# Optimization experiments

Hardware: AMD Instinct MI355X
Metric: run time of the kernel (lower is better)

The kernel has to match this reference:

```python
import jax, jax.numpy as jnp
import numpy as np

ND, PD, NH = 256, 128, 8   # node_dim, pair_dim, n_head
HD = ND // NH              # head_dim = 32
N, L = 1, 256


def _inorm(x):
    # InstanceNorm2d (affine=False), x is NHWC: normalize per (N,C) over H,W
    m = jnp.mean(x, axis=(1, 2), keepdims=True)
    v = jnp.var(x, axis=(1, 2), keepdims=True)
    return (x - m) * jax.lax.rsqrt(v + 1e-5)


def _conv3x3(x, w, b):
    # w in torch OIHW layout -> HWIO; stride 1, padding 1 ('SAME')
    y = jax.lax.conv_general_dilated(x, jnp.transpose(w, (2, 3, 1, 0)), (1, 1), 'SAME',
                                     dimension_numbers=('NHWC', 'HWIO', 'NHWC'))
    return y + b


def _lrelu(x):
    return jnp.where(x >= 0, x, 0.01 * x)


def _ln(x, g, b):
    m = jnp.mean(x, axis=-1, keepdims=True)
    v = jnp.var(x, axis=-1, keepdims=True)
    return (x - m) * jax.lax.rsqrt(v + 1e-5) * g + b


def setup_inputs() -> dict:
    key = jax.random.key(0)
    ks = jax.random.split(key, 16)
    rn = lambda k, s: jax.random.normal(k, s, jnp.float32) * 0.02
    return dict(
        x=jax.random.normal(ks[0], (N, L, ND), jnp.float32),
        z=jax.random.normal(ks[1], (N, L, L, PD), jnp.float32),
        plddt=jax.random.uniform(ks[2], (N, L, L, 1), jnp.float32),
        Wq=rn(ks[3], (ND, ND)), Wk=rn(ks[4], (ND, ND)), Wv=rn(ks[5], (ND, ND)),
        Wp2a=rn(ks[6], (NH, PD)),
        conv_a_w=rn(ks[7], (NH, 2 * NH, 3, 3)), conv_a_b=jnp.zeros((NH,), jnp.float32),
        conv_p_w=rn(ks[8], (NH, NH + 1, 3, 3)), conv_p_b=jnp.zeros((NH,), jnp.float32),
        ln1_g=jnp.ones((NH * PD + ND,), jnp.float32), ln1_b=jnp.zeros((NH * PD + ND,), jnp.float32),
        lin1_w=rn(ks[9], (2 * ND, NH * PD + ND)), lin1_b=jnp.zeros((2 * ND,), jnp.float32),
        ln2_g=jnp.ones((2 * ND,), jnp.float32), ln2_b=jnp.zeros((2 * ND,), jnp.float32),
        lin2_w=rn(ks[10], (ND, 2 * ND)), lin2_b=jnp.zeros((ND,), jnp.float32),
        lnf_g=jnp.ones((ND,), jnp.float32), lnf_b=jnp.zeros((ND,), jnp.float32),
        conv_z_w=rn(ks[11], (PD, NH + PD, 3, 3)), conv_z_b=jnp.zeros((PD,), jnp.float32),
    )


def reference(x, z, plddt, Wq, Wk, Wv, Wp2a, conv_a_w, conv_a_b, conv_p_w, conv_p_b,
              ln1_g, ln1_b, lin1_w, lin1_b, ln2_g, ln2_b, lin2_w, lin2_b,
              lnf_g, lnf_b, conv_z_w, conv_z_b):
    n, l, _ = x.shape
    inv_sqrt_hd = np.float32(1.0 / np.sqrt(HD))
    # _node2alpha: per-head QK^T / sqrt(head_dim) -> (N,L,L,H)
    q = (x @ Wq.T).reshape(n, l, NH, HD)
    k = (x @ Wk.T).reshape(n, l, NH, HD)
    v = (x @ Wv.T).reshape(n, l, NH, HD)
    a_node = jnp.einsum('nihd,njhd->nijh', q, k) * inv_sqrt_hd
    # _pair2alpha
    a_pair = z @ Wp2a.T  # (N,L,L,H)
    # conv2dalpha: cat(pair, node) channels-last, InstanceNorm + Conv3x3 + LeakyReLU
    alpha = _lrelu(_conv3x3(_inorm(jnp.concatenate([a_pair, a_node], axis=-1)), conv_a_w, conv_a_b))
    # alpha_mask_plddt
    alpha = _lrelu(_conv3x3(_inorm(jnp.concatenate([alpha, plddt], axis=-1)), conv_p_w, conv_p_b))
    # _node_aggregation: (N,L,H,hd) head-major flatten -> (N,L,node_dim)
    node_from_node = jnp.einsum('nijh,njhd->nihd', alpha, v).reshape(n, l, ND)
    # _pair_aggregation: direct contraction over j (avoids (N,L,L,H,P) blowup)
    node_from_pair = jnp.einsum('nijh,nijp->nihp', alpha, z).reshape(n, l, NH * PD)
    # out_transform: LN -> Linear -> LN -> LeakyReLU -> Linear
    h = jnp.concatenate([node_from_pair, node_from_node], axis=-1)
    h = _ln(h, ln1_g, ln1_b)
    h = _ln(h @ lin1_w.T + lin1_b, ln2_g, ln2_b)
    x_out = _lrelu(h) @ lin2_w.T + lin2_b
    x_new = _ln(x + x_out, lnf_g, lnf_b)
    # alpha2pair
    z_new = _lrelu(_conv3x3(_inorm(jnp.concatenate([z, alpha], axis=-1)), conv_z_w, conv_z_b))
    return x_new, z_new
```

## Files before the change

### kernel.cpp

```cpp
#include <hip/hip_runtime.h>
#include <math.h>

#define LLEN 256
#define NDIM 256
#define NHEAD 8
#define HDIM 32
#define NPIX (LLEN*LLEN)

typedef __bf16 bf16x8 __attribute__((ext_vector_type(8)));
typedef float f32x4 __attribute__((ext_vector_type(4)));

constexpr size_t OFF_Q     = 0;
constexpr size_t OFF_K     = 65536;
constexpr size_t OFF_V     = 131072;
constexpr size_t OFF_CAT16 = 196608;
constexpr size_t OFF_H1B   = 196608;
constexpr size_t OFF_W1B   = 360448;
constexpr size_t OFF_A1    = 1245184;
constexpr size_t OFF_ALPHA = 1769472;
constexpr size_t OFF_AGG   = 2293760;
constexpr size_t OFF_Y     = 2621440;
constexpr size_t OFF_ST16  = 2752512;
constexpr size_t OFF_ST9   = 2752544;
constexpr size_t OFF_ST136 = 2752576;
constexpr size_t OFF_PART  = 2752864;
constexpr size_t OFF_PART2 = 2892128;
constexpr size_t OFF_WZB2  = 3031392;

__device__ inline unsigned short f2b(float x){
  union { float f; unsigned u; } a; a.f = x;
  unsigned r = a.u + 0x7fffu + ((a.u >> 16) & 1u);
  return (unsigned short)(r >> 16);
}

__global__ __launch_bounds__(256) void qkv_kernel(
    const float* __restrict__ x, const float* __restrict__ Wq,
    const float* __restrict__ Wk, const float* __restrict__ Wv,
    float* __restrict__ q, float* __restrict__ k, float* __restrict__ v){
  __shared__ __align__(16) float xs[8][256];
  int t = threadIdx.x;
  int i0 = blockIdx.x * 8;
  int m = blockIdx.y;
  const float* W = (m==0)?Wq:((m==1)?Wk:Wv);
  float* out = (m==0)?q:((m==1)?k:v);
  for (int idx = t; idx < 2048; idx += 256)
    xs[idx>>8][idx&255] = x[(size_t)i0*256 + idx];
  __syncthreads();
  float acc[8];
  #pragma unroll
  for (int r = 0; r < 8; r++) acc[r] = 0.f;
  const float4* wr = (const float4*)(W + (size_t)t*256);
  for (int kk = 0; kk < 64; ++kk){
    float4 w4 = wr[kk];
    #pragma unroll
    for (int r = 0; r < 8; r++){
      float4 xv = ((const float4*)xs[r])[kk];
      acc[r] += w4.x*xv.x + w4.y*xv.y + w4.z*xv.z + w4.w*xv.w;
    }
  }
  #pragma unroll
  for (int r = 0; r < 8; r++) out[(size_t)(i0+r)*256 + t] = acc[r];
}

__global__ __launch_bounds__(256) void cat16v3_kernel(
    const float* __restrict__ z, const float* __restrict__ qb,
    const float* __restrict__ kb, const float* __restrict__ Wp2a,
    float* __restrict__ cat16){
  __shared__ __align__(16) float zs2[32*132];
  __shared__ __align__(16) float ws2[8*132];
  int t = threadIdx.x;
  int pix0 = blockIdx.x * 32;
  int i = pix0 >> 8;
  int j0 = pix0 & 255;
  {
    int h = t >> 5, j = t & 31;
    float4 v = *(const float4*)(Wp2a + h*128 + j*4);
    *(float4*)(ws2 + h*132 + j*4) = v;
  }
  #pragma unroll
  for (int k = 0; k < 4; ++k){
    int idx = t + k*256;
    int pix = idx >> 5, j = idx & 31;
    float4 v = *(const float4*)(z + ((size_t)(pix0 + pix))*128 + j*4);
    *(float4*)(zs2 + pix*132 + j*4) = v;
  }
  __syncthreads();
  int p8 = t >> 3, h = t & 7;
  const float* zr = zs2 + p8*132;
  const float* wr = ws2 + h*132;
  float ap = 0.f;
  #pragma unroll 8
  for (int j = 0; j < 32; ++j){
    float4 a = *(const float4*)(zr + j*4);
    float4 b = *(const float4*)(wr + j*4);
    ap += a.x*b.x + a.y*b.y + a.z*b.z + a.w*b.w;
  }
  const float* qg = qb + (size_t)i*256 + h*32;
  const float* kg = kb + (size_t)(j0 + p8)*256 + h*32;
  float an = 0.f;
  #pragma unroll
  for (int d4 = 0; d4 < 8; ++d4){
    float4 a = *(const float4*)(qg + d4*4);
    float4 b = *(const float4*)(kg + d4*4);
    an += a.x*b.x + a.y*b.y + a.z*b.z + a.w*b.w;
  }
  an *= 0.17677669529663689f;
  int pix = pix0 + p8;
  cat16[(size_t)pix*16 + h] = ap;
  cat16[(size_t)pix*16 + 8 + h] = an;
}

__global__ __launch_bounds__(256) void statsA_z_kernel(
    const float* __restrict__ z, float* __restrict__ part, float* __restrict__ part2){
  __shared__ float4 sm[256], sq[256];
  int t = threadIdx.x, b = blockIdx.x;
  int c4 = t & 31, po = t >> 5;
  float4 s = {0,0,0,0}, q = {0,0,0,0};
  for (int g = 0; g < 8; ++g){
    int px = b*64 + po + g*8;
    float4 v = *(const float4*)(z + (size_t)px*128 + c4*4);
    s.x += v.x; s.y += v.y; s.z += v.z; s.w += v.w;
    q.x += v.x*v.x; q.y += v.y*v.y; q.z += v.z*v.z; q.w += v.w*v.w;
  }
  sm[t] = s; sq[t] = q;
  __syncthreads();
  if (t < 32){
    float4 S = sm[t], Q = sq[t];
    for (int p2 = 1; p2 < 8; ++p2){
      float4 a = sm[p2*32 + t], c = sq[p2*32 + t];
      S.x += a.x; S.y += a.y; S.z += a.z; S.w += a.w;
      Q.x += c.x; Q.y += c.y; Q.z += c.z; Q.w += c.w;
    }
    part [(size_t)(t*4+0)*1024 + b] = S.x; part [(size_t)(t*4+1)*1024 + b] = S.y;
    part [(size_t)(t*4+2)*1024 + b] = S.z; part [(size_t)(t*4+3)*1024 + b] = S.w;
    part2[(size_t)(t*4+0)*1024 + b] = Q.x; part2[(size_t)(t*4+1)*1024 + b] = Q.y;
    part2[(size_t)(t*4+2)*1024 + b] = Q.z; part2[(size_t)(t*4+3)*1024 + b] = Q.w;
  }
}

__global__ __launch_bounds__(256) void statsA_16_kernel(
    const float* __restrict__ src, float* __restrict__ part, float* __restrict__ part2){
  __shared__ float4 sm[256], sq[256];
  int t = threadIdx.x, b = blockIdx.x;
  int c4 = t & 3, po = t >> 2;
  float4 s = {0,0,0,0}, q = {0,0,0,0};
  for (int g = 0; g < 4; ++g){
    int px = b*256 + po + g*64;
    float4 v = *(const float4*)(src + (size_t)px*16 + c4*4);
    s.x += v.x; s.y += v.y; s.z += v.z; s.w += v.w;
    q.x += v.x*v.x; q.y += v.y*v.y; q.z += v.z*v.z; q.w += v.w*v.w;
  }
  sm[t] = s; sq[t] = q;
  __syncthreads();
  if (t < 4){
    float4 S = sm[t], Q = sq[t];
    for (int p2 = 1; p2 < 64; ++p2){
      float4 a = sm[p2*4 + t], c = sq[p2*4 + t];
      S.x += a.x; S.y += a.y; S.z += a.z; S.w += a.w;
      Q.x += c.x; Q.y += c.y; Q.z += c.z; Q.w += c.w;
    }
    part [(size_t)(t*4+0)*1024 + b] = S.x; part [(size_t)(t*4+1)*1024 + b] = S.y;
    part [(size_t)(t*4+2)*1024 + b] = S.z; part [(size_t)(t*4+3)*1024 + b] = S.w;
    part2[(size_t)(t*4+0)*1024 + b] = Q.x; part2[(size_t)(t*4+1)*1024 + b] = Q.y;
    part2[(size_t)(t*4+2)*1024 + b] = Q.z; part2[(size_t)(t*4+3)*1024 + b] = Q.w;
  }
}

__global__ __launch_bounds__(256) void statsA_s8_kernel(
    const float* __restrict__ src, float* __restrict__ part, float* __restrict__ part2,
    int coff){
  __shared__ float sm[256], sq[256];
  int t = threadIdx.x, b = blockIdx.x;
  int ch = t & 7, po = t >> 3;
  float s = 0.f, q = 0.f;
  for (int g = 0; g < 8; ++g){
    int px = b*256 + po + g*32;
    float v = src[(size_t)px*8 + ch];
    s += v; q += v*v;
  }
  sm[t] = s; sq[t] = q;
  __syncthreads();
  if (t < 8){
    float S = 0.f, Q = 0.f;
    for (int p2 = 0; p2 < 32; ++p2){ S += sm[p2*8 + t]; Q += sq[p2*8 + t]; }
    part [(size_t)(coff+t)*1024 + b] = S;
    part2[(size_t)(coff+t)*1024 + b] = Q;
  }
}

__device__ inline void block_reduce2(float& s, float& s2, float* red){
  int t = threadIdx.x;
  int lane = t & 63, wv = t >> 6;
  #pragma unroll
  for (int o = 32; o > 0; o >>= 1){ s += __shfl_down(s, o); s2 += __shfl_down(s2, o); }
  __syncthreads();
  if (lane == 0){ red[wv] = s; red[4+wv] = s2; }
  __syncthreads();
  s  = red[0]+red[1]+red[2]+red[3];
  s2 = red[4]+red[5]+red[6]+red[7];
}

__global__ __launch_bounds__(256) void statsA_s1_kernel(
    const float* __restrict__ src, float* __restrict__ part, float* __restrict__ part2,
    int coff){
  __shared__ float red[8];
  int t = threadIdx.x, b = blockIdx.x;
  float v = src[(size_t)b*256 + t];
  float s = v, q = v*v;
  block_reduce2(s, q, red);
  if (t == 0){ part[(size_t)coff*1024 + b] = s; part2[(size_t)coff*1024 + b] = q; }
}

__global__ __launch_bounds__(256) void statsB_kernel(
    const float* __restrict__ part, const float* __restrict__ part2,
    float* __restrict__ st, int C, int csplit, int nb_main, int nb_tail){
  __shared__ float red[8];
  int c = blockIdx.x, t = threadIdx.x;
  int nb = (c < csplit) ? nb_main : nb_tail;
  float s = 0.f, q = 0.f;
  for (int i = t; i < nb; i += 256){ s += part[(size_t)c*1024 + i]; q += part2[(size_t)c*1024 + i]; }
  block_reduce2(s, q, red);
  if (t == 0){
    float m = s * (1.f/NPIX);
    float var = q * (1.f/NPIX) - m*m;
    st[c] = m;
    st[C + c] = rsqrtf(var + 1e-5f);
  }
}

template<int CIN, int COUT>
__global__ __launch_bounds__(256) void conv_small5_kernel(
    const float* __restrict__ A, int Ca, const float* __restrict__ B, int Cb,
    const float* __restrict__ st, const float* __restrict__ w,
    const float* __restrict__ bias, float* __restrict__ out){
  constexpr int WD = 67;
  __shared__ float xn[3][CIN][WD];
  __shared__ float wsm[COUT*CIN*9];
  __shared__ float ms[CIN], isd[CIN], bs[COUT];
  int t = threadIdx.x;
  int i = blockIdx.x >> 2, chb = blockIdx.x & 3;
  int c0 = chb*64;
  if (t < CIN){ ms[t] = st[t]; isd[t] = st[CIN + t]; }
  if (t < COUT) bs[t] = bias[t];
  for (int idx = t; idx < COUT*CIN*9; idx += 256) wsm[idx] = w[idx];
  __syncthreads();
  constexpr int TOT = 66*CIN;
  for (int s = 0; s < 3; ++s){
    int ir = i - 1 + s;
    for (int idx = t; idx < TOT; idx += 256){
      int col = idx / CIN, c = idx - col*CIN;
      int gcol = c0 + col - 1;
      float vv = 0.f;
      if (ir >= 0 && ir < 256 && gcol >= 0 && gcol < 256){
        size_t pix = (size_t)ir*256 + gcol;
        float raw = (c < Ca) ? A[pix*Ca + c] : B[pix*Cb + (c - Ca)];
        vv = (raw - ms[c]) * isd[c];
      }
      xn[s][c][col] = vv;
    }
  }
  __syncthreads();
  int os = t >> 6, tc = t & 63;
  float a0 = bs[os*2], a1 = bs[os*2 + 1];
  #pragma unroll
  for (int kh = 0; kh < 3; ++kh){
    #pragma unroll
    for (int c = 0; c < CIN; ++c){
      float x0 = xn[kh][c][tc];
      float x1 = xn[kh][c][tc + 1];
      float x2 = xn[kh][c][tc + 2];
      const float* w0 = wsm + (((os*2+0)*CIN + c)*3 + kh)*3;
      const float* w1 = wsm + (((os*2+1)*CIN + c)*3 + kh)*3;
      a0 += x0*w0[0] + x1*w0[1] + x2*w0[2];
      a1 += x0*w1[0] + x1*w1[1] + x2*w1[2];
    }
  }
  a0 = (a0 >= 0.f) ? a0 : 0.01f*a0;
  a1 = (a1 >= 0.f) ? a1 : 0.01f*a1;
  float2 v2 = { a0, a1 };
  *(float2*)(out + ((size_t)(i*256 + c0 + tc))*COUT + os*2) = v2;
}

__global__ __launch_bounds__(512) void agg_kernel2(
    const float* __restrict__ alpha, const float* __restrict__ z,
    const float* __restrict__ v, float* __restrict__ agg){
  __shared__ float as[2048];
  __shared__ float pp[256][4];
  __shared__ float np[256];
  int i = blockIdx.x, t = threadIdx.x;
  for (int idx = t; idx < 2048; idx += 512) as[idx] = alpha[(size_t)i*2048 + idx];
  __syncthreads();
  int tt = t & 255, jh = t >> 8;
  int p = tt & 127, hh = tt >> 7;
  const float* zrow = z + (size_t)i*32768 + (size_t)jh*128*128;
  const float* ar0 = as + jh*128*8;
  float a0=0.f, a1=0.f, a2=0.f, a3=0.f;
  #pragma unroll 8
  for (int j = 0; j < 128; ++j){
    float zv = zrow[j*128 + p];
    const float* ar = ar0 + j*8 + hh*4;
    a0 += ar[0]*zv; a1 += ar[1]*zv; a2 += ar[2]*zv; a3 += ar[3]*zv;
  }
  int h = tt >> 5;
  float an = 0.f;
  const float* vrow = v + (size_t)jh*128*256;
  const float* ah0 = as + jh*128*8;
  #pragma unroll 8
  for (int j = 0; j < 128; ++j) an += ah0[j*8 + h]*vrow[j*256 + tt];
  if (jh == 1){
    pp[tt][0]=a0; pp[tt][1]=a1; pp[tt][2]=a2; pp[tt][3]=a3; np[tt]=an;
  }
  __syncthreads();
  if (jh == 0){
    a0 += pp[tt][0]; a1 += pp[tt][1]; a2 += pp[tt][2]; a3 += pp[tt][3];
    an += np[tt];
    size_t ob = (size_t)i*1280;
    agg[ob + (hh*4+0)*128 + p] = a0;
    agg[ob + (hh*4+1)*128 + p] = a1;
    agg[ob + (hh*4+2)*128 + p] = a2;
    agg[ob + (hh*4+3)*128 + p] = a3;
    agg[ob + 1024 + tt] = an;
  }
}

__global__ __launch_bounds__(256) void ln1_kernel(
    const float* __restrict__ agg,
    const float* __restrict__ ln1_g, const float* __restrict__ ln1_b,
    unsigned short* __restrict__ h1b){
  __shared__ float red[8];
  int i = blockIdx.x, t = threadIdx.x;
  float v[5], s = 0.f, s2 = 0.f;
  #pragma unroll
  for (int qq = 0; qq < 5; ++qq){
    v[qq] = agg[(size_t)i*1280 + qq*256 + t];
    s += v[qq]; s2 += v[qq]*v[qq];
  }
  block_reduce2(s, s2, red);
  float m = s*(1.f/1280.f), istd = rsqrtf(s2*(1.f/1280.f) - m*m + 1e-5f);
  #pragma unroll
  for (int qq = 0; qq < 5; ++qq){
    int kk = qq*256 + t;
    h1b[(size_t)i*1280 + kk] = f2b((v[qq] - m)*istd*ln1_g[kk] + ln1_b[kk]);
  }
}

__global__ __launch_bounds__(256) void w1_prep(const float* __restrict__ w,
                                               unsigned short* __restrict__ wb){
  int idx = (blockIdx.x*256 + threadIdx.x)*4;
  float4 v = *(const float4*)(w + idx);
  ushort4 u;
  u.x = f2b(v.x); u.y = f2b(v.y); u.z = f2b(v.z); u.w = f2b(v.w);
  *(ushort4*)(wb + idx) = u;
}

__global__ __launch_bounds__(256) void gemm1_kernel(
    const unsigned short* __restrict__ h1b, const unsigned short* __restrict__ w1b,
    const float* __restrict__ lin1_b, float* __restrict__ y){
  int t = threadIdx.x;
  int mb = blockIdx.x & 3, nb = blockIdx.x >> 2;
  int lane = t & 63, w = t >> 6;
  int li = lane & 15, lg = lane >> 4;
  int mh = w & 1, nh = w >> 1;
  int mbase = mb*64 + mh*32, nbase = nb*64 + nh*32;
  f32x4 acc[2][2];
  #pragma unroll
  for (int a = 0; a < 2; ++a)
    #pragma unroll
    for (int b = 0; b < 2; ++b) acc[a][b] = (f32x4){0.f,0.f,0.f,0.f};
  const unsigned short* ar0 = h1b + (size_t)(mbase + li)*1280 + lg*8;
  const unsigned short* ar1 = ar0 + 16*1280;
  const unsigned short* br0 = w1b + (size_t)(nbase + li)*1280 + lg*8;
  const unsigned short* br1 = br0 + 16*1280;
  #pragma unroll 4
  for (int ks = 0; ks < 40; ++ks){
    bf16x8 a0 = *(const bf16x8*)(ar0 + ks*32);
    bf16x8 a1 = *(const bf16x8*)(ar1 + ks*32);
    bf16x8 b0 = *(const bf16x8*)(br0 + ks*32);
    bf16x8 b1 = *(const bf16x8*)(br1 + ks*32);
    acc[0][0] = __builtin_amdgcn_mfma_f32_16x16x32_bf16(a0, b0, acc[0][0], 0,0,0);
    acc[0][1] = __builtin_amdgcn_mfma_f32_16x16x32_bf16(a0, b1, acc[0][1], 0,0,0);
    acc[1][0] = __builtin_amdgcn_mfma_f32_16x16x32_bf16(a1, b0, acc[1][0], 0,0,0);
    acc[1][1] = __builtin_amdgcn_mfma_f32_16x16x32_bf16(a1, b1, acc[1][1], 0,0,0);
  }
  #pragma unroll
  for (int mi = 0; mi < 2; ++mi){
    #pragma unroll
    for (int ni = 0; ni < 2; ++ni){
      int col = nbase + ni*16 + li;
      float bb = lin1_b[col];
      #pragma unroll
      for (int ri = 0; ri < 4; ++ri){
        int row = mbase + mi*16 + lg*4 + ri;
        y[(size_t)row*512 + col] = acc[mi][ni][ri] + bb;
      }
    }
  }
}

__global__ __launch_bounds__(256) void outB2_kernel(
    const float* __restrict__ y, const float* __restrict__ x,
    const float* __restrict__ ln2_g, const float* __restrict__ ln2_b,
    const float* __restrict__ lin2_w, const float* __restrict__ lin2_b,
    const float* __restrict__ lnf_g, const float* __restrict__ lnf_b,
    float* __restrict__ xout){
  __shared__ __align__(16) float h2[2][512];
  __shared__ float red[8];
  int t = threadIdx.x;
  int rb = blockIdx.x;
  for (int r = 0; r < 2; ++r){
    int i = rb*2 + r;
    float y0 = y[(size_t)i*512 + t], y1 = y[(size_t)i*512 + 256 + t];
    float s = y0 + y1, s2 = y0*y0 + y1*y1;
    block_reduce2(s, s2, red);
    float m = s*(1.f/512.f), istd = rsqrtf(s2*(1.f/512.f) - m*m + 1e-5f);
    float z0 = (y0 - m)*istd*ln2_g[t] + ln2_b[t];
    float z1 = (y1 - m)*istd*ln2_g[t+256] + ln2_b[t+256];
    h2[r][t]     = (z0 >= 0.f) ? z0 : 0.01f*z0;
    h2[r][t+256] = (z1 >= 0.f) ? z1 : 0.01f*z1;
  }
  __syncthreads();
  float acc[2];
  acc[0] = 0.f; acc[1] = 0.f;
  const float4* wr = (const float4*)(lin2_w + (size_t)t*512);
  #pragma unroll 4
  for (int kk = 0; kk < 128; ++kk){
    float4 w4 = wr[kk];
    #pragma unroll
    for (int r = 0; r < 2; ++r){
      float4 h = ((const float4*)h2[r])[kk];
      acc[r] += w4.x*h.x + w4.y*h.y + w4.z*h.z + w4.w*h.w;
    }
  }
  float bb = lin2_b[t];
  for (int r = 0; r < 2; ++r){
    int i = rb*2 + r;
    float xr = x[(size_t)i*256 + t] + acc[r] + bb;
    float s = xr, s2 = xr*xr;
    block_reduce2(s, s2, red);
    float m = s*(1.f/256.f), istd = rsqrtf(s2*(1.f/256.f) - m*m + 1e-5f);
    xout[(size_t)i*256 + t] = (xr - m)*istd*lnf_g[t] + lnf_b[t];
  }
}

__global__ __launch_bounds__(256) void wz_prep2(const float* __restrict__ w,
                                                unsigned short* __restrict__ wzb2){
  int idx = blockIdx.x*256 + threadIdx.x;
  if (idx >= 23040) return;
  int lane = idx & 63;
  int f = idx >> 6;
  int k = f % 5; int ft = f / 5; int tap = ft % 9; int ocb = ft / 9;
  int oc = ocb*16 + (lane & 15);
  int chb = k*32 + (lane >> 4)*8;
  unsigned short u[8];
  #pragma unroll
  for (int j = 0; j < 8; ++j){
    int ch = chb + j;
    float vv = (ch < 136) ? w[(size_t)oc*1224 + ch*9 + tap] : 0.f;
    u[j] = f2b(vv);
  }
  uint4 pk;
  pk.x = (unsigned)u[0] | ((unsigned)u[1]<<16);
  pk.y = (unsigned)u[2] | ((unsigned)u[3]<<16);
  pk.z = (unsigned)u[4] | ((unsigned)u[5]<<16);
  pk.w = (unsigned)u[6] | ((unsigned)u[7]<<16);
  *(uint4*)(wzb2 + (size_t)idx*8) = pk;
}

__global__ __launch_bounds__(256) void conv_z7_kernel(
    const float* __restrict__ z, const float* __restrict__ alpha,
    const float* __restrict__ st, const unsigned short* __restrict__ wzb2,
    const float* __restrict__ bias, float* __restrict__ out){
  __shared__ __align__(16) unsigned short xs[4*578*8];
  __shared__ float msp[153], isp[153];
  int t = threadIdx.x;
  int stripe = blockIdx.x & 7, rg = blockIdx.x >> 3;
  int i0 = rg*2, c0 = stripe*32;
  int lane = t & 63, w = t >> 6;
  int li = lane & 15, lg = lane >> 4;
  int wocb = w*2;
  if (t < 153){
    int cq = t/9, j = t - cq*9;
    bool vld = (j < 8);
    int ch = cq*8 + j;
    msp[t] = vld ? st[ch] : 0.f;
    isp[t] = vld ? st[136 + ch] : 0.f;
  }
  __syncthreads();
  for (int it = 0; it < 3; ++it){
    int cidx = t + it*256;
    int col = cidx / 17, cq = cidx - col*17;
    int gcol = c0 + col - 1;
    float mm[8], ss[8];
    #pragma unroll
    for (int j = 0; j < 8; ++j){ mm[j] = msp[cq*9 + j]; ss[j] = isp[cq*9 + j]; }
    if (cidx < 578){
      #pragma unroll
      for (int s = 0; s < 4; ++s){
        int ir = i0 - 1 + s;
        uint4 pk = {0u,0u,0u,0u};
        if (ir >= 0 && ir < 256 && gcol >= 0 && gcol < 256){
          const float* src = (cq < 16) ? (z + ((size_t)ir*256 + gcol)*128 + cq*8)
                                       : (alpha + ((size_t)ir*256 + gcol)*8);
          float4 r0 = *(const float4*)src;
          float4 r1 = *(const float4*)(src + 4);
          unsigned short u0 = f2b((r0.x - mm[0])*ss[0]);
          unsigned short u1 = f2b((r0.y - mm[1])*ss[1]);
          unsigned short u2 = f2b((r0.z - mm[2])*ss[2]);
          unsigned short u3 = f2b((r0.w - mm[3])*ss[3]);
          unsigned short u4 = f2b((r1.x - mm[4])*ss[4]);
          unsigned short u5 = f2b((r1.y - mm[5])*ss[5]);
          unsigned short u6 = f2b((r1.z - mm[6])*ss[6]);
          unsigned short u7 = f2b((r1.w - mm[7])*ss[7]);
          pk.x = (unsigned)u0 | ((unsigned)u1<<16);
          pk.y = (unsigned)u2 | ((unsigned)u3<<16);
          pk.z = (unsigned)u4 | ((unsigned)u5<<16);
          pk.w = (unsigned)u6 | ((unsigned)u7<<16);
        }
        *(uint4*)(xs + ((size_t)(s*578 + cidx))*8) = pk;
      }
    }
  }
  __syncthreads();

  f32x4 acc[2][2][2];
  #pragma unroll
  for (int r = 0; r < 2; ++r)
    #pragma unroll
    for (int m = 0; m < 2; ++m)
      #pragma unroll
      for (int o = 0; o < 2; ++o) acc[r][m][o] = (f32x4){0.f,0.f,0.f,0.f};

  for (int kh = 0; kh < 3; ++kh){
    for (int kw = 0; kw < 3; ++kw){
      int tap = kh*3 + kw;
      bf16x8 wf[5][2];
      #pragma unroll
      for (int k = 0; k < 5; ++k)
        #pragma unroll
        for (int o = 0; o < 2; ++o)
          wf[k][o] = *(const bf16x8*)(wzb2 + (size_t)((((wocb+o)*9 + tap)*5 + k)*64 + lane)*8);
      #pragma unroll
      for (int r = 0; r < 2; ++r){
        const unsigned short* sb = xs + (size_t)(r + kh)*578*8;
        #pragma unroll
        for (int k = 0; k < 5; ++k){
          int cq = (k < 4) ? (k*4 + lg) : 16;
          bf16x8 a0 = *(const bf16x8*)(sb + ((li+kw)*17 + cq)*8);
          bf16x8 a1 = *(const bf16x8*)(sb + ((li+kw+16)*17 + cq)*8);
          acc[r][0][0] = __builtin_amdgcn_mfma_f32_16x16x32_bf16(a0, wf[k][0], acc[r][0][0], 0,0,0);
          acc[r][0][1] = __builtin_amdgcn_mfma_f32_16x16x32_bf16(a0, wf[k][1], acc[r][0][1], 0,0,0);
          acc[r][1][0] = __builtin_amdgcn_mfma_f32_16x16x32_bf16(a1, wf[k][0], acc[r][1][0], 0,0,0);
          acc[r][1][1] = __builtin_amdgcn_mfma_f32_16x16x32_bf16(a1, wf[k][1], acc[r][1][1], 0,0,0);
        }
      }
    }
  }

  float b0 = bias[wocb*16 + li];
  float b1 = bias[(wocb+1)*16 + li];
  #pragma unroll
  for (int r = 0; r < 2; ++r){
    int i = i0 + r;
    #pragma unroll
    for (int m = 0; m < 2; ++m){
      #pragma unroll
      for (int ri = 0; ri < 4; ++ri){
        int px = m*16 + lg*4 + ri;
        size_t obase = ((size_t)(i*256 + c0 + px))*128;
        float v0 = acc[r][m][0][ri] + b0;
        float v1 = acc[r][m][1][ri] + b1;
        v0 = (v0 >= 0.f) ? v0 : 0.01f*v0;
        v1 = (v1 >= 0.f) ? v1 : 0.01f*v1;
        out[obase + wocb*16 + li]     = v0;
        out[obase + (wocb+1)*16 + li] = v1;
      }
    }
  }
}

extern "C" void kernel_launch(void* const* d_in, const int* in_sizes, int n_in,
                              void* d_out, int out_size, void* d_ws, size_t ws_size,
                              hipStream_t stream){
  const float* x        = (const float*)d_in[0];
  const float* z        = (const float*)d_in[1];
  const float* plddt    = (const float*)d_in[2];
  const float* Wq       = (const float*)d_in[3];
  const float* Wk       = (const float*)d_in[4];
  const float* Wv       = (const float*)d_in[5];
  const float* Wp2a     = (const float*)d_in[6];
  const float* conv_a_w = (const float*)d_in[7];
  const float* conv_a_b = (const float*)d_in[8];
  const float* conv_p_w = (const float*)d_in[9];
  const float* conv_p_b = (const float*)d_in[10];
  const float* ln1_g    = (const float*)d_in[11];
  const float* ln1_b    = (const float*)d_in[12];
  const float* lin1_w   = (const float*)d_in[13];
  const float* lin1_b   = (const float*)d_in[14];
  const float* ln2_g    = (const float*)d_in[15];
  const float* ln2_b    = (const float*)d_in[16];
  const float* lin2_w   = (const float*)d_in[17];
  const float* lin2_b   = (const float*)d_in[18];
  const float* lnf_g    = (const float*)d_in[19];
  const float* lnf_b    = (const float*)d_in[20];
  const float* conv_z_w = (const float*)d_in[21];
  const float* conv_z_b = (const float*)d_in[22];

  float* ws    = (float*)d_ws;
  float* q     = ws + OFF_Q;
  float* k     = ws + OFF_K;
  float* v     = ws + OFF_V;
  float* cat16 = ws + OFF_CAT16;
  float* a1    = ws + OFF_A1;
  float* alpha = ws + OFF_ALPHA;
  float* agg   = ws + OFF_AGG;
  float* y     = ws + OFF_Y;
  float* st16  = ws + OFF_ST16;
  float* st9   = ws + OFF_ST9;
  float* st136 = ws + OFF_ST136;
  float* part  = ws + OFF_PART;
  float* part2 = ws + OFF_PART2;
  unsigned short* wzb2 = (unsigned short*)(ws + OFF_WZB2);
  unsigned short* h1b  = (unsigned short*)(ws + OFF_H1B);
  unsigned short* w1b  = (unsigned short*)(ws + OFF_W1B);

  float* xout = (float*)d_out;
  float* zout = (float*)d_out + 65536;

  qkv_kernel<<<dim3(32,3), 256, 0, stream>>>(x, Wq, Wk, Wv, q, k, v);
  cat16v3_kernel<<<2048, 256, 0, stream>>>(z, q, k, Wp2a, cat16);
  statsA_16_kernel<<<256, 256, 0, stream>>>(cat16, part, part2);
  statsB_kernel<<<16, 256, 0, stream>>>(part, part2, st16, 16, 16, 256, 256);
  conv_small5_kernel<16,8><<<1024, 256, 0, stream>>>(cat16, 16, (const float*)nullptr, 0,
                                                     st16, conv_a_w, conv_a_b, a1);
  statsA_s8_kernel<<<256, 256, 0, stream>>>(a1, part, part2, 0);
  statsA_s1_kernel<<<256, 256, 0, stream>>>(plddt, part, part2, 8);
  statsB_kernel<<<9, 256, 0, stream>>>(part, part2, st9, 9, 9, 256, 256);
  conv_small5_kernel<9,8><<<1024, 256, 0, stream>>>(a1, 8, plddt, 1,
                                                    st9, conv_p_w, conv_p_b, alpha);
  agg_kernel2<<<256, 512, 0, stream>>>(alpha, z, v, agg);
  w1_prep<<<640, 256, 0, stream>>>(lin1_w, w1b);
  ln1_kernel<<<256, 256, 0, stream>>>(agg, ln1_g, ln1_b, h1b);
  gemm1_kernel<<<32, 256, 0, stream>>>(h1b, w1b, lin1_b, y);
  outB2_kernel<<<128, 256, 0, stream>>>(y, x, ln2_g, ln2_b, lin2_w, lin2_b,
                                        lnf_g, lnf_b, xout);
  statsA_z_kernel<<<1024, 256, 0, stream>>>(z, part, part2);
  statsA_s8_kernel<<<256, 256, 0, stream>>>(alpha, part, part2, 128);
  statsB_kernel<<<136, 256, 0, stream>>>(part, part2, st136, 136, 128, 1024, 256);
  wz_prep2<<<90, 256, 0, stream>>>(conv_z_w, wzb2);
  conv_z7_kernel<<<1024, 256, 0, stream>>>(z, alpha, st136, wzb2, conv_z_b, zout);
}
```

Baseline: 189.6 us.

## Fuse instance-norm partial statistics into producer kernels, drop separate stats passes

Per-block partial sums and squared sums for instance norm are now computed inside the cat16 and small-conv kernels from shared-memory tiles, instead of in separate statsA kernels that reread the intermediates. This removes four launches and their reads of cat16, a1, alpha and plddt. It adds a block barrier and a short serial reduction to the producer kernels. The scratch buffer for p16 is aliased onto the y region, which is safe only if y is written later.

Result: faster. 183.6 us (-3.2%).

```diff
diff --git a/kernel.cpp b/kernel.cpp
--- a/kernel.cpp
+++ b/kernel.cpp
@@ -62,21 +62,20 @@
   for (int r = 0; r < 8; r++) out[(size_t)(i0+r)*256 + t] = acc[r];
 }
 
-__global__ __launch_bounds__(256) void cat16v3_kernel(
+__global__ __launch_bounds__(256) void cat16v4_kernel(
     const float* __restrict__ z, const float* __restrict__ qb,
     const float* __restrict__ kb, const float* __restrict__ Wp2a,
-    float* __restrict__ cat16){
+    float* __restrict__ cat16, float* __restrict__ p16, float* __restrict__ p16q){
   __shared__ __align__(16) float zs2[32*132];
   __shared__ __align__(16) float ws2[8*132];
+  __shared__ float sA[512];
   int t = threadIdx.x;
   int pix0 = blockIdx.x * 32;
   int i = pix0 >> 8;
   int j0 = pix0 & 255;
-  {
-    int h = t >> 5, j = t & 31;
+  { int h = t >> 5, j = t & 31;
     float4 v = *(const float4*)(Wp2a + h*128 + j*4);
-    *(float4*)(ws2 + h*132 + j*4) = v;
-  }
+    *(float4*)(ws2 + h*132 + j*4) = v; }
   #pragma unroll
   for (int k = 0; k < 4; ++k){
     int idx = t + k*256;
@@ -108,6 +107,16 @@
   int pix = pix0 + p8;
   cat16[(size_t)pix*16 + h] = ap;
   cat16[(size_t)pix*16 + 8 + h] = an;
+  sA[p8*16 + h] = ap;
+  sA[p8*16 + 8 + h] = an;
+  __syncthreads();
+  if (t < 16){
+    float S = 0.f, Q = 0.f;
+    #pragma unroll
+    for (int p = 0; p < 32; ++p){ float v = sA[p*16 + t]; S += v; Q += v*v; }
+    p16 [(size_t)t*2048 + blockIdx.x] = S;
+    p16q[(size_t)t*2048 + blockIdx.x] = Q;
+  }
 }
 
 __global__ __launch_bounds__(256) void statsA_z_kernel(
@@ -138,56 +147,6 @@
   }
 }
 
-__global__ __launch_bounds__(256) void statsA_16_kernel(
-    const float* __restrict__ src, float* __restrict__ part, float* __restrict__ part2){
-  __shared__ float4 sm[256], sq[256];
-  int t = threadIdx.x, b = blockIdx.x;
-  int c4 = t & 3, po = t >> 2;
-  float4 s = {0,0,0,0}, q = {0,0,0,0};
-  for (int g = 0; g < 4; ++g){
-    int px = b*256 + po + g*64;
-    float4 v = *(const float4*)(src + (size_t)px*16 + c4*4);
-    s.x += v.x; s.y += v.y; s.z += v.z; s.w += v.w;
-    q.x += v.x*v.x; q.y += v.y*v.y; q.z += v.z*v.z; q.w += v.w*v.w;
-  }
-  sm[t] = s; sq[t] = q;
-  __syncthreads();
-  if (t < 4){
-    float4 S = sm[t], Q = sq[t];
-    for (int p2 = 1; p2 < 64; ++p2){
-      float4 a = sm[p2*4 + t], c = sq[p2*4 + t];
-      S.x += a.x; S.y += a.y; S.z += a.z; S.w += a.w;
-      Q.x += c.x; Q.y += c.y; Q.z += c.z; Q.w += c.w;
-    }
-    part [(size_t)(t*4+0)*1024 + b] = S.x; part [(size_t)(t*4+1)*1024 + b] = S.y;
-    part [(size_t)(t*4+2)*1024 + b] = S.z; part [(size_t)(t*4+3)*1024 + b] = S.w;
-    part2[(size_t)(t*4+0)*1024 + b] = Q.x; part2[(size_t)(t*4+1)*1024 + b] = Q.y;
-    part2[(size_t)(t*4+2)*1024 + b] = Q.z; part2[(size_t)(t*4+3)*1024 + b] = Q.w;
-  }
-}
-
-__global__ __launch_bounds__(256) void statsA_s8_kernel(
-    const float* __restrict__ src, float* __restrict__ part, float* __restrict__ part2,
-    int coff){
-  __shared__ float sm[256], sq[256];
-  int t = threadIdx.x, b = blockIdx.x;
-  int ch = t & 7, po = t >> 3;
-  float s = 0.f, q = 0.f;
-  for (int g = 0; g < 8; ++g){
-    int px = b*256 + po + g*32;
-    float v = src[(size_t)px*8 + ch];
-    s += v; q += v*v;
-  }
-  sm[t] = s; sq[t] = q;
-  __syncthreads();
-  if (t < 8){
-    float S = 0.f, Q = 0.f;
-    for (int p2 = 0; p2 < 32; ++p2){ S += sm[p2*8 + t]; Q += sq[p2*8 + t]; }
-    part [(size_t)(coff+t)*1024 + b] = S;
-    part2[(size_t)(coff+t)*1024 + b] = Q;
-  }
-}
-
 __device__ inline void block_reduce2(float& s, float& s2, float* red){
   int t = threadIdx.x;
   int lane = t & 63, wv = t >> 6;
@@ -200,25 +159,16 @@
   s2 = red[4]+red[5]+red[6]+red[7];
 }
 
-__global__ __launch_bounds__(256) void statsA_s1_kernel(
-    const float* __restrict__ src, float* __restrict__ part, float* __restrict__ part2,
-    int coff){
-  __shared__ float red[8];
-  int t = threadIdx.x, b = blockIdx.x;
-  float v = src[(size_t)b*256 + t];
-  float s = v, q = v*v;
-  block_reduce2(s, q, red);
-  if (t == 0){ part[(size_t)coff*1024 + b] = s; part2[(size_t)coff*1024 + b] = q; }
-}
-
 __global__ __launch_bounds__(256) void statsB_kernel(
     const float* __restrict__ part, const float* __restrict__ part2,
-    float* __restrict__ st, int C, int csplit, int nb_main, int nb_tail){
+    float* __restrict__ st, int C, int nb, int stride){
   __shared__ float red[8];
   int c = blockIdx.x, t = threadIdx.x;
-  int nb = (c < csplit) ? nb_main : nb_tail;
   float s = 0.f, q = 0.f;
-  for (int i = t; i < nb; i += 256){ s += part[(size_t)c*1024 + i]; q += part2[(size_t)c*1024 + i]; }
+  for (int i = t; i < nb; i += 256){
+    s += part[(size_t)c*stride + i];
+    q += part2[(size_t)c*stride + i];
+  }
   block_reduce2(s, q, red);
   if (t == 0){
     float m = s * (1.f/NPIX);
@@ -228,15 +178,19 @@
   }
 }
 
-template<int CIN, int COUT>
-__global__ __launch_bounds__(256) void conv_small5_kernel(
+template<int CIN, int COUT, bool PL>
+__global__ __launch_bounds__(256) void conv_small6_kernel(
     const float* __restrict__ A, int Ca, const float* __restrict__ B, int Cb,
     const float* __restrict__ st, const float* __restrict__ w,
-    const float* __restrict__ bias, float* __restrict__ out){
+    const float* __restrict__ bias, float* __restrict__ out,
+    const float* __restrict__ plddt, float* __restrict__ part,
+    float* __restrict__ part2, int coff){
   constexpr int WD = 67;
   __shared__ float xn[3][CIN][WD];
   __shared__ float wsm[COUT*CIN*9];
   __shared__ float ms[CIN], isd[CIN], bs[COUT];
+  __shared__ float sB[COUT*64];
+  __shared__ float sP[64];
   int t = threadIdx.x;
   int i = blockIdx.x >> 2, chb = blockIdx.x & 3;
   int c0 = chb*64;
@@ -279,6 +233,25 @@
   a1 = (a1 >= 0.f) ? a1 : 0.01f*a1;
   float2 v2 = { a0, a1 };
   *(float2*)(out + ((size_t)(i*256 + c0 + tc))*COUT + os*2) = v2;
+  sB[os*128 + tc]      = a0;
+  sB[os*128 + 64 + tc] = a1;
+  if (PL && t < 64) sP[t] = plddt[(size_t)i*256 + c0 + t];
+  __syncthreads();
+  if (t < COUT){
+    int os2 = t >> 1, par = t & 1;
+    const float* src = sB + os2*128 + par*64;
+    float S = 0.f, Q = 0.f;
+    #pragma unroll
+    for (int j = 0; j < 64; ++j){ float v = src[j]; S += v; Q += v*v; }
+    part [(size_t)(coff + t)*1024 + blockIdx.x] = S;
+    part2[(size_t)(coff + t)*1024 + blockIdx.x] = Q;
+  } else if (PL && t == COUT){
+    float S = 0.f, Q = 0.f;
+    #pragma unroll
+    for (int j = 0; j < 64; ++j){ float v = sP[j]; S += v; Q += v*v; }
+    part [(size_t)(coff + COUT)*1024 + blockIdx.x] = S;
+    part2[(size_t)(coff + COUT)*1024 + blockIdx.x] = Q;
+  }
 }
 
 __global__ __launch_bounds__(512) void agg_kernel2(
@@ -614,6 +587,8 @@
   float* alpha = ws + OFF_ALPHA;
   float* agg   = ws + OFF_AGG;
   float* y     = ws + OFF_Y;
+  float* p16   = ws + OFF_Y;
+  float* p16q  = ws + OFF_Y + 32768;
   float* st16  = ws + OFF_ST16;
   float* st9   = ws + OFF_ST9;
   float* st136 = ws + OFF_ST136;
@@ -627,16 +602,15 @@
   float* zout = (float*)d_out + 65536;
 
   qkv_kernel<<<dim3(32,3), 256, 0, stream>>>(x, Wq, Wk, Wv, q, k, v);
-  cat16v3_kernel<<<2048, 256, 0, stream>>>(z, q, k, Wp2a, cat16);
-  statsA_16_kernel<<<256, 256, 0, stream>>>(cat16, part, part2);
-  statsB_kernel<<<16, 256, 0, stream>>>(part, part2, st16, 16, 16, 256, 256);
-  conv_small5_kernel<16,8><<<1024, 256, 0, stream>>>(cat16, 16, (const float*)nullptr, 0,
-                                                     st16, conv_a_w, conv_a_b, a1);
-  statsA_s8_kernel<<<256, 256, 0, stream>>>(a1, part, part2, 0);
-  statsA_s1_kernel<<<256, 256, 0, stream>>>(plddt, part, part2, 8);
-  statsB_kernel<<<9, 256, 0, stream>>>(part, part2, st9, 9, 9, 256, 256);
-  conv_small5_kernel<9,8><<<1024, 256, 0, stream>>>(a1, 8, plddt, 1,
-                                                    st9, conv_p_w, conv_p_b, alpha);
+  cat16v4_kernel<<<2048, 256, 0, stream>>>(z, q, k, Wp2a, cat16, p16, p16q);
+  statsB_kernel<<<16, 256, 0, stream>>>(p16, p16q, st16, 16, 2048, 2048);
+  conv_small6_kernel<16,8,true><<<1024, 256, 0, stream>>>(
+      cat16, 16, (const float*)nullptr, 0, st16, conv_a_w, conv_a_b, a1,
+      plddt, part, part2, 0);
+  statsB_kernel<<<9, 256, 0, stream>>>(part, part2, st9, 9, 1024, 1024);
+  conv_small6_kernel<9,8,false><<<1024, 256, 0, stream>>>(
+      a1, 8, plddt, 1, st9, conv_p_w, conv_p_b, alpha,
+      (const float*)nullptr, part, part2, 128);
   agg_kernel2<<<256, 512, 0, stream>>>(alpha, z, v, agg);
   w1_prep<<<640, 256, 0, stream>>>(lin1_w, w1b);
   ln1_kernel<<<256, 256, 0, stream>>>(agg, ln1_g, ln1_b, h1b);
@@ -644,8 +618,7 @@
   outB2_kernel<<<128, 256, 0, stream>>>(y, x, ln2_g, ln2_b, lin2_w, lin2_b,
                                         lnf_g, lnf_b, xout);
   statsA_z_kernel<<<1024, 256, 0, stream>>>(z, part, part2);
-  statsA_s8_kernel<<<256, 256, 0, stream>>>(alpha, part, part2, 128);
-  statsB_kernel<<<136, 256, 0, stream>>>(part, part2, st136, 136, 128, 1024, 256);
+  statsB_kernel<<<136, 256, 0, stream>>>(part, part2, st136, 136, 1024, 1024);
   wz_prep2<<<90, 256, 0, stream>>>(conv_z_w, wzb2);
   conv_z7_kernel<<<1024, 256, 0, stream>>>(z, alpha, st136, wzb2, conv_z_b, zout);
 }
```
